# Optimization experiments

Measured on AMD Instinct MI355X. Metric: run time of the kernel, lower is better.

The kernel has to match this reference:

```python
import jax, jax.numpy as jnp
import numpy as np

B, T, L, D, U = 2048, 500, 128, 64, 128  # batch, time steps, latent_dim, output_dim, n_units


def setup_inputs() -> dict:
    key = jax.random.key(0)
    ks = jax.random.split(key, 10)
    def init(k, shape, fan_in):
        return jax.random.uniform(k, shape, jnp.float32, -1.0, 1.0) / np.sqrt(fan_in)
    return {
        "first_point": jax.random.normal(ks[0], (1, B, L), jnp.float32),
        "time_steps_to_predict": jnp.arange(T, dtype=jnp.float32),
        # GRUCell params (torch layout: weight [3*hidden, in], gates ordered r,z,n)
        "w_ih": init(ks[1], (3 * L, D + 1), L),
        "w_hh": init(ks[2], (3 * L, L), L),
        "b_ih": init(ks[3], (3 * L,), L),
        "b_hh": init(ks[4], (3 * L,), L),
        # output_net: Linear(L,U) -> tanh -> Linear(U,D)
        "w1": init(ks[5], (U, L), L),
        "b1": jnp.zeros((U,), jnp.float32),
        "w2": init(ks[6], (D, U), U),
        "b2": jnp.zeros((D,), jnp.float32),
    }


def _gru_cell(x, h, w_ih, w_hh, b_ih, b_hh):
    gi = x @ w_ih.T + b_ih  # [B, 3L]
    gh = h @ w_hh.T + b_hh  # [B, 3L]
    i_r, i_z, i_n = jnp.split(gi, 3, axis=-1)
    h_r, h_z, h_n = jnp.split(gh, 3, axis=-1)
    r = jax.nn.sigmoid(i_r + h_r)
    z = jax.nn.sigmoid(i_z + h_z)
    n = jnp.tanh(i_n + r * h_n)
    return (1.0 - z) * n + z * h


def reference(first_point, time_steps_to_predict, w_ih, w_hh, b_ih, b_hh, w1, b1, w2, b2):
    def mlp(h):
        return jnp.tanh(h @ w1.T + b1) @ w2.T + b2  # [B, D]

    ts = time_steps_to_predict
    delta_ts = jnp.concatenate([jnp.zeros((1,), ts.dtype), ts[1:] - ts[:-1]])  # [T]

    h0 = first_point[0]          # [B, L]
    p0 = mlp(h0)                 # [B, D]
    batch = h0.shape[0]

    def step(carry, dt):
        h, p = carry
        dt_col = jnp.broadcast_to(dt.reshape(1, 1), (batch, 1))
        x = jnp.concatenate([p, dt_col], axis=-1)  # [B, D+1]
        h = _gru_cell(x, h, w_ih, w_hh, b_ih, b_hh)
        p = mlp(h)
        return (h, p), (h, p)

    _, (hs, ps) = jax.lax.scan(step, (h0, p0), delta_ts[1:])  # [T-1, B, *]
    sol_z = jnp.concatenate([h0[None], hs], axis=0)   # [T, B, L]
    pred_x = jnp.concatenate([p0[None], ps], axis=0)  # [T, B, D]
    sol_z = jnp.transpose(sol_z, (1, 0, 2))[None]     # [1, B, T, L]
    pred_x = jnp.transpose(pred_x, (1, 0, 2))[None]   # [1, B, T, D]
    return sol_z, pred_x
```

## Files before the change

kernel.cpp:

```cpp
#include <hip/hip_runtime.h>

#define BB 2048
#define TT 500
#define LL 128
#define DD 64
#define UU 128

using f16x8 = __attribute__((ext_vector_type(8))) _Float16;
using f32x4 = __attribute__((ext_vector_type(4))) float;

__device__ __forceinline__ float bf2f(unsigned short u){
  union { unsigned u; float f; } v; v.u = ((unsigned)u) << 16; return v.f;
}
__device__ __forceinline__ unsigned short f2bf(float f){
  union { float f; unsigned u; } v; v.f = f;
  unsigned r = v.u + 0x7FFFu + ((v.u >> 16) & 1u);
  return (unsigned short)(r >> 16);
}
__device__ __forceinline__ float cvt(unsigned short v){ return bf2f(v); }
__device__ __forceinline__ float cvt(float v){ return v; }

__device__ __forceinline__ float sigmoidf_(float x){
  return __builtin_amdgcn_rcpf(1.f + __expf(-x));
}
__device__ __forceinline__ float tanhf_(float x){
  float e = __expf(2.f * x);
  return 1.f - 2.f * __builtin_amdgcn_rcpf(1.f + e);
}

__device__ __forceinline__ void bar_lds(){
  asm volatile("s_waitcnt lgkmcnt(0)\n\ts_barrier" ::: "memory");
}

#define SH 136
#define SA 136

struct Frags {
  f16x8 Wc[3][4];
  f16x8 Wh[3][4];
  f16x8 W1f[4];
  f16x8 W2f[4];
  float br, bz, bin, bhn, wdr, wdz, wdn, b1c, b2c;
};

template <typename T>
__device__ __forceinline__ void preload(
    const void* wih_, const void* whh_, const void* bih_, const void* bhh_,
    const void* w1_, const void* b1_, const void* w2_, const void* b2_,
    int c, int lq, Frags& F)
{
  const T* wih = (const T*)wih_; const T* whh = (const T*)whh_;
  const T* bih = (const T*)bih_; const T* bhh = (const T*)bhh_;
  const T* w1  = (const T*)w1_;  const T* b1  = (const T*)b1_;
  const T* w2  = (const T*)w2_;  const T* b2  = (const T*)b2_;
  #pragma unroll
  for (int g = 0; g < 3; ++g){
    const int row = g*128 + c;
    #pragma unroll
    for (int kt = 0; kt < 4; ++kt)
      #pragma unroll
      for (int j = 0; j < 8; ++j)
        F.Wh[g][kt][j] = (_Float16)cvt(whh[row*128 + kt*32 + lq*8 + j]);
  }
  #pragma unroll
  for (int kt = 0; kt < 4; ++kt)
    #pragma unroll
    for (int j = 0; j < 8; ++j)
      F.W1f[kt][j] = (_Float16)cvt(w1[c*128 + kt*32 + lq*8 + j]);
  const int c2 = c & 63;
  #pragma unroll
  for (int kt = 0; kt < 4; ++kt)
    #pragma unroll
    for (int j = 0; j < 8; ++j)
      F.W2f[kt][j] = (_Float16)cvt(w2[c2*128 + kt*32 + lq*8 + j]);

  for (int kt = 0; kt < 4; ++kt){
    float acc[3][8];
    #pragma unroll
    for (int g = 0; g < 3; ++g)
      #pragma unroll
      for (int j = 0; j < 8; ++j) acc[g][j] = 0.f;
    for (int d = 0; d < 64; ++d){
      float w2r[8];
      #pragma unroll
      for (int j = 0; j < 8; ++j)
        w2r[j] = cvt(w2[d*128 + kt*32 + lq*8 + j]);
      #pragma unroll
      for (int g = 0; g < 3; ++g){
        const float wpv = cvt(wih[(g*128 + c)*65 + d]);
        #pragma unroll
        for (int j = 0; j < 8; ++j) acc[g][j] += wpv * w2r[j];
      }
    }
    #pragma unroll
    for (int g = 0; g < 3; ++g)
      #pragma unroll
      for (int j = 0; j < 8; ++j)
        F.Wc[g][kt][j] = (_Float16)acc[g][j];
  }
  float bc[3] = {0.f, 0.f, 0.f};
  for (int d = 0; d < 64; ++d){
    const float b2v = cvt(b2[d]);
    #pragma unroll
    for (int g = 0; g < 3; ++g)
      bc[g] += cvt(wih[(g*128 + c)*65 + d]) * b2v;
  }
  F.br  = cvt(bih[c])     + cvt(bhh[c])     + bc[0];
  F.bz  = cvt(bih[128+c]) + cvt(bhh[128+c]) + bc[1];
  F.bin = cvt(bih[256+c]) + bc[2];
  F.bhn = cvt(bhh[256+c]);
  F.wdr = cvt(wih[c*65 + 64]);
  F.wdz = cvt(wih[(128+c)*65 + 64]);
  F.wdn = cvt(wih[(256+c)*65 + 64]);
  F.b1c = cvt(b1[c]);
  F.b2c = cvt(b2[c2]);
}

__global__ __launch_bounds__(512, 2) void rnn_decoder(
    const void* __restrict__ fp0,
    const void* __restrict__ ts,
    const void* __restrict__ wih,
    const void* __restrict__ whh,
    const void* __restrict__ bih,
    const void* __restrict__ bhh,
    const void* __restrict__ w1,
    const void* __restrict__ b1,
    const void* __restrict__ w2,
    const void* __restrict__ b2,
    void* __restrict__ out)
{
  __shared__ __align__(16) _Float16 sh[16*SH];
  __shared__ __align__(16) _Float16 sa[16*SA];
  __shared__ float dts[TT];

  const int tid  = threadIdx.x;
  const int wv   = tid >> 6;
  const int lane = tid & 63;
  const int lm   = lane & 15;
  const int lq   = lane >> 4;
  const int b0   = blockIdx.x << 4;
  const int c    = (wv << 4) + lm;

  const bool isbf = (((const unsigned*)ts)[1] != 0x3F800000u);

  Frags F;
  if (isbf) preload<unsigned short>(wih, whh, bih, bhh, w1, b1, w2, b2, c, lq, F);
  else      preload<float>         (wih, whh, bih, bhh, w1, b1, w2, b2, c, lq, F);

  if (isbf){
    const unsigned short* t16 = (const unsigned short*)ts;
    for (int t = tid; t < TT; t += 512)
      dts[t] = t ? (bf2f(t16[t]) - bf2f(t16[t-1])) : 0.f;
  } else {
    const float* t32 = (const float*)ts;
    for (int t = tid; t < TT; t += 512)
      dts[t] = t ? (t32[t] - t32[t-1]) : 0.f;
  }

  unsigned short* outh16 = (unsigned short*)out;
  unsigned short* outp16 = outh16 + (size_t)BB*TT*LL;
  float* outh32 = (float*)out;
  float* outp32 = outh32 + (size_t)BB*TT*LL;

  {
    const int row = tid >> 5;
    const int k4  = (tid & 31) << 2;
    if (isbf){
      const unsigned short* src = (const unsigned short*)fp0 + (b0 + row)*LL + k4;
      ushort4 v = *(const ushort4*)src;
      #pragma unroll
      for (int j = 0; j < 4; ++j)
        sh[row*SH + k4 + j] = (_Float16)bf2f(((const unsigned short*)&v)[j]);
      *(ushort4*)(outh16 + (size_t)(b0 + row)*TT*LL + k4) = v;
    } else {
      const float* src = (const float*)fp0 + (b0 + row)*LL + k4;
      float4 v = *(const float4*)src;
      sh[row*SH + k4 + 0] = (_Float16)v.x;
      sh[row*SH + k4 + 1] = (_Float16)v.y;
      sh[row*SH + k4 + 2] = (_Float16)v.z;
      sh[row*SH + k4 + 3] = (_Float16)v.w;
      *(float4*)(outh32 + (size_t)(b0 + row)*TT*LL + k4) = v;
    }
  }
  bar_lds();

  float hprev[4];
  #pragma unroll
  for (int i = 0; i < 4; ++i)
    hprev[i] = (float)sh[(lq*4 + i)*SH + c];

  f16x8 ahc[4], aac[4];
  #pragma unroll
  for (int kt = 0; kt < 4; ++kt)
    ahc[kt] = *(const f16x8*)&sh[lm*SH + kt*32 + lq*8];

  {
    f32x4 acc = {0,0,0,0};
    #pragma unroll
    for (int kt = 0; kt < 4; ++kt)
      acc = __builtin_amdgcn_mfma_f32_16x16x32_f16(ahc[kt], F.W1f[kt], acc, 0,0,0);
    #pragma unroll
    for (int i = 0; i < 4; ++i)
      sa[(lq*4 + i)*SA + c] = (_Float16)tanhf_(acc[i] + F.b1c);
  }
  bar_lds();
  #pragma unroll
  for (int kt = 0; kt < 4; ++kt)
    aac[kt] = *(const f16x8*)&sa[lm*SA + kt*32 + lq*8];

  for (int t = 1; t < TT; ++t){
    const float dt = dts[t];
    f32x4 aR = {0,0,0,0}, aZ = {0,0,0,0}, aN = {0,0,0,0}, aH = {0,0,0,0};
    #pragma unroll
    for (int kt = 0; kt < 4; ++kt){
      aR = __builtin_amdgcn_mfma_f32_16x16x32_f16(aac[kt], F.Wc[0][kt], aR, 0,0,0);
      aZ = __builtin_amdgcn_mfma_f32_16x16x32_f16(aac[kt], F.Wc[1][kt], aZ, 0,0,0);
      aN = __builtin_amdgcn_mfma_f32_16x16x32_f16(aac[kt], F.Wc[2][kt], aN, 0,0,0);
      aH = __builtin_amdgcn_mfma_f32_16x16x32_f16(ahc[kt], F.Wh[2][kt], aH, 0,0,0);
    }
    #pragma unroll
    for (int kt = 0; kt < 4; ++kt){
      aR = __builtin_amdgcn_mfma_f32_16x16x32_f16(ahc[kt], F.Wh[0][kt], aR, 0,0,0);
      aZ = __builtin_amdgcn_mfma_f32_16x16x32_f16(ahc[kt], F.Wh[1][kt], aZ, 0,0,0);
    }
    f32x4 aP = {0,0,0,0};
    if (wv < 4){
      #pragma unroll
      for (int kt = 0; kt < 4; ++kt)
        aP = __builtin_amdgcn_mfma_f32_16x16x32_f16(aac[kt], F.W2f[kt], aP, 0,0,0);
    }
    float hnew[4];
    #pragma unroll
    for (int i = 0; i < 4; ++i){
      const float r = sigmoidf_(aR[i] + F.br + dt*F.wdr);
      const float z = sigmoidf_(aZ[i] + F.bz + dt*F.wdz);
      const float n = tanhf_(aN[i] + F.bin + dt*F.wdn + r*(aH[i] + F.bhn));
      hnew[i] = (1.f - z)*n + z*hprev[i];
      hprev[i] = hnew[i];
    }
    #pragma unroll
    for (int i = 0; i < 4; ++i)
      sh[(lq*4 + i)*SH + c] = (_Float16)hnew[i];
    bar_lds();
    #pragma unroll
    for (int kt = 0; kt < 4; ++kt)
      ahc[kt] = *(const f16x8*)&sh[lm*SH + kt*32 + lq*8];
    if (!isbf){
      #pragma unroll
      for (int i = 0; i < 4; ++i)
        outh32[(size_t)(b0 + lq*4 + i)*TT*LL + (size_t)t*LL + c] = hnew[i];
      if (wv < 4){
        #pragma unroll
        for (int i = 0; i < 4; ++i)
          outp32[(size_t)(b0 + lq*4 + i)*TT*DD + (size_t)(t-1)*DD + c] = aP[i] + F.b2c;
      }
    } else {
      #pragma unroll
      for (int i = 0; i < 4; ++i)
        outh16[(size_t)(b0 + lq*4 + i)*TT*LL + (size_t)t*LL + c] = f2bf(hnew[i]);
      if (wv < 4){
        #pragma unroll
        for (int i = 0; i < 4; ++i)
          outp16[(size_t)(b0 + lq*4 + i)*TT*DD + (size_t)(t-1)*DD + c] = f2bf(aP[i] + F.b2c);
      }
    }
    {
      f32x4 acc = {0,0,0,0};
      #pragma unroll
      for (int kt = 0; kt < 4; ++kt)
        acc = __builtin_amdgcn_mfma_f32_16x16x32_f16(ahc[kt], F.W1f[kt], acc, 0,0,0);
      #pragma unroll
      for (int i = 0; i < 4; ++i)
        sa[(lq*4 + i)*SA + c] = (_Float16)tanhf_(acc[i] + F.b1c);
    }
    bar_lds();
    #pragma unroll
    for (int kt = 0; kt < 4; ++kt)
      aac[kt] = *(const f16x8*)&sa[lm*SA + kt*32 + lq*8];
  }

  if (wv < 4){
    f32x4 aP = {0,0,0,0};
    #pragma unroll
    for (int kt = 0; kt < 4; ++kt)
      aP = __builtin_amdgcn_mfma_f32_16x16x32_f16(aac[kt], F.W2f[kt], aP, 0,0,0);
    if (!isbf){
      #pragma unroll
      for (int i = 0; i < 4; ++i)
        outp32[(size_t)(b0 + lq*4 + i)*TT*DD + (size_t)(TT-1)*DD + c] = aP[i] + F.b2c;
    } else {
      #pragma unroll
      for (int i = 0; i < 4; ++i)
        outp16[(size_t)(b0 + lq*4 + i)*TT*DD + (size_t)(TT-1)*DD + c] = f2bf(aP[i] + F.b2c);
    }
  }
}

extern "C" void kernel_launch(void* const* d_in, const int* in_sizes, int n_in,
                              void* d_out, int out_size, void* d_ws, size_t ws_size,
                              hipStream_t stream) {
  (void)in_sizes; (void)n_in; (void)out_size; (void)d_ws; (void)ws_size;
  rnn_decoder<<<dim3(BB/16), dim3(512), 0, stream>>>(
      d_in[0],
      d_in[1],
      d_in[2],
      d_in[3],
      d_in[4],
      d_in[5],
      d_in[6],
      d_in[7],
      d_in[8],
      d_in[9],
      d_out);
}
```

Baseline: 1.342 ms.

## Fold exp2 scaling into weights, move hidden GEMMs off the critical path, precompute output offsets

The log2(e) factors of sigmoid and tanh are folded into the preloaded weights and biases, so each activation becomes a raw v_exp_f32 plus a reciprocal with no multiply. The hidden-state MFMAs (r, z, n gates) for the next step now run right after the new h is read back, alongside the W1 MLP, rather than at the start of the next step, shortening the dependency chain between the two barriers. Output addresses are held as incremented 32-bit offsets instead of being recomputed each step. Scaling weights before the fp16 conversion changes rounding slightly, and 32-bit offsets assume the output index stays within range.

```diff
diff --git a/kernel.cpp b/kernel.cpp
--- a/kernel.cpp
+++ b/kernel.cpp
@@ -20,17 +20,16 @@
 __device__ __forceinline__ float cvt(unsigned short v){ return bf2f(v); }
 __device__ __forceinline__ float cvt(float v){ return v; }
 
-__device__ __forceinline__ float sigmoidf_(float x){
-  return __builtin_amdgcn_rcpf(1.f + __expf(-x));
-}
-__device__ __forceinline__ float tanhf_(float x){
-  float e = __expf(2.f * x);
-  return 1.f - 2.f * __builtin_amdgcn_rcpf(1.f + e);
+__device__ __forceinline__ float exp2_(float x){
+  float r; asm("v_exp_f32 %0, %1" : "=v"(r) : "v"(x)); return r;
 }
 
 __device__ __forceinline__ void bar_lds(){
   asm volatile("s_waitcnt lgkmcnt(0)\n\ts_barrier" ::: "memory");
 }
+
+#define C1 (-1.44269504088896340736f)
+#define C2 ( 2.88539008177792681472f)
 
 #define SH 136
 #define SA 136
@@ -53,6 +52,7 @@
   const T* bih = (const T*)bih_; const T* bhh = (const T*)bhh_;
   const T* w1  = (const T*)w1_;  const T* b1  = (const T*)b1_;
   const T* w2  = (const T*)w2_;  const T* b2  = (const T*)b2_;
+  const float gs[3] = {C1, C1, C2};
   #pragma unroll
   for (int g = 0; g < 3; ++g){
     const int row = g*128 + c;
@@ -60,13 +60,13 @@
     for (int kt = 0; kt < 4; ++kt)
       #pragma unroll
       for (int j = 0; j < 8; ++j)
-        F.Wh[g][kt][j] = (_Float16)cvt(whh[row*128 + kt*32 + lq*8 + j]);
+        F.Wh[g][kt][j] = (_Float16)(gs[g]*cvt(whh[row*128 + kt*32 + lq*8 + j]));
   }
   #pragma unroll
   for (int kt = 0; kt < 4; ++kt)
     #pragma unroll
     for (int j = 0; j < 8; ++j)
-      F.W1f[kt][j] = (_Float16)cvt(w1[c*128 + kt*32 + lq*8 + j]);
+      F.W1f[kt][j] = (_Float16)(C2*cvt(w1[c*128 + kt*32 + lq*8 + j]));
   const int c2 = c & 63;
   #pragma unroll
   for (int kt = 0; kt < 4; ++kt)
@@ -96,7 +96,7 @@
     for (int g = 0; g < 3; ++g)
       #pragma unroll
       for (int j = 0; j < 8; ++j)
-        F.Wc[g][kt][j] = (_Float16)acc[g][j];
+        F.Wc[g][kt][j] = (_Float16)(gs[g]*acc[g][j]);
   }
   float bc[3] = {0.f, 0.f, 0.f};
   for (int d = 0; d < 64; ++d){
@@ -105,14 +105,14 @@
     for (int g = 0; g < 3; ++g)
       bc[g] += cvt(wih[(g*128 + c)*65 + d]) * b2v;
   }
-  F.br  = cvt(bih[c])     + cvt(bhh[c])     + bc[0];
-  F.bz  = cvt(bih[128+c]) + cvt(bhh[128+c]) + bc[1];
-  F.bin = cvt(bih[256+c]) + bc[2];
-  F.bhn = cvt(bhh[256+c]);
-  F.wdr = cvt(wih[c*65 + 64]);
-  F.wdz = cvt(wih[(128+c)*65 + 64]);
-  F.wdn = cvt(wih[(256+c)*65 + 64]);
-  F.b1c = cvt(b1[c]);
+  F.br  = C1*(cvt(bih[c])     + cvt(bhh[c])     + bc[0]);
+  F.bz  = C1*(cvt(bih[128+c]) + cvt(bhh[128+c]) + bc[1]);
+  F.bin = C2*(cvt(bih[256+c]) + bc[2]);
+  F.bhn = C2*cvt(bhh[256+c]);
+  F.wdr = C1*cvt(wih[c*65 + 64]);
+  F.wdz = C1*cvt(wih[(128+c)*65 + 64]);
+  F.wdn = C2*cvt(wih[(256+c)*65 + 64]);
+  F.b1c = C2*cvt(b1[c]);
   F.b2c = cvt(b2[c2]);
 }
 
@@ -162,6 +162,13 @@
   float* outh32 = (float*)out;
   float* outp32 = outh32 + (size_t)BB*TT*LL;
 
+  unsigned offh[4], offp[4];
+  #pragma unroll
+  for (int i = 0; i < 4; ++i){
+    offh[i] = (unsigned)((b0 + lq*4 + i)*TT*LL + c) + (unsigned)LL;
+    offp[i] = (unsigned)((b0 + lq*4 + i)*TT*DD + (c & 63));
+  }
+
   {
     const int row = tid >> 5;
     const int k4  = (tid & 31) << 2;
@@ -194,14 +201,22 @@
   for (int kt = 0; kt < 4; ++kt)
     ahc[kt] = *(const f16x8*)&sh[lm*SH + kt*32 + lq*8];
 
+  f32x4 aR = {0,0,0,0}, aZ = {0,0,0,0}, aH = {0,0,0,0};
   {
     f32x4 acc = {0,0,0,0};
     #pragma unroll
     for (int kt = 0; kt < 4; ++kt)
       acc = __builtin_amdgcn_mfma_f32_16x16x32_f16(ahc[kt], F.W1f[kt], acc, 0,0,0);
     #pragma unroll
+    for (int kt = 0; kt < 4; ++kt){
+      aR = __builtin_amdgcn_mfma_f32_16x16x32_f16(ahc[kt], F.Wh[0][kt], aR, 0,0,0);
+      aZ = __builtin_amdgcn_mfma_f32_16x16x32_f16(ahc[kt], F.Wh[1][kt], aZ, 0,0,0);
+      aH = __builtin_amdgcn_mfma_f32_16x16x32_f16(ahc[kt], F.Wh[2][kt], aH, 0,0,0);
+    }
+    #pragma unroll
     for (int i = 0; i < 4; ++i)
-      sa[(lq*4 + i)*SA + c] = (_Float16)tanhf_(acc[i] + F.b1c);
+      sa[(lq*4 + i)*SA + c] =
+        (_Float16)(1.f - 2.f*__builtin_amdgcn_rcpf(1.f + exp2_(acc[i] + F.b1c)));
   }
   bar_lds();
   #pragma unroll
@@ -210,69 +225,75 @@
 
   for (int t = 1; t < TT; ++t){
     const float dt = dts[t];
-    f32x4 aR = {0,0,0,0}, aZ = {0,0,0,0}, aN = {0,0,0,0}, aH = {0,0,0,0};
+    f32x4 aN = {0,0,0,0};
     #pragma unroll
     for (int kt = 0; kt < 4; ++kt){
       aR = __builtin_amdgcn_mfma_f32_16x16x32_f16(aac[kt], F.Wc[0][kt], aR, 0,0,0);
       aZ = __builtin_amdgcn_mfma_f32_16x16x32_f16(aac[kt], F.Wc[1][kt], aZ, 0,0,0);
       aN = __builtin_amdgcn_mfma_f32_16x16x32_f16(aac[kt], F.Wc[2][kt], aN, 0,0,0);
-      aH = __builtin_amdgcn_mfma_f32_16x16x32_f16(ahc[kt], F.Wh[2][kt], aH, 0,0,0);
-    }
+    }
+    f32x4 aP = {0,0,0,0};
+    if (wv < 4){
+      #pragma unroll
+      for (int kt = 0; kt < 4; ++kt)
+        aP = __builtin_amdgcn_mfma_f32_16x16x32_f16(aac[kt], F.W2f[kt], aP, 0,0,0);
+    }
+    const float rb = F.br + dt*F.wdr;
+    const float zb = F.bz + dt*F.wdz;
+    const float nb = F.bin + dt*F.wdn;
+    float hnew[4];
+    #pragma unroll
+    for (int i = 0; i < 4; ++i){
+      const float r = __builtin_amdgcn_rcpf(1.f + exp2_(aR[i] + rb));
+      const float z = __builtin_amdgcn_rcpf(1.f + exp2_(aZ[i] + zb));
+      const float y = aN[i] + nb + r*(aH[i] + F.bhn);
+      const float n = 1.f - 2.f*__builtin_amdgcn_rcpf(1.f + exp2_(y));
+      hnew[i] = n + z*(hprev[i] - n);
+      hprev[i] = hnew[i];
+    }
+    #pragma unroll
+    for (int i = 0; i < 4; ++i)
+      sh[(lq*4 + i)*SH + c] = (_Float16)hnew[i];
+    bar_lds();
+    #pragma unroll
+    for (int kt = 0; kt < 4; ++kt)
+      ahc[kt] = *(const f16x8*)&sh[lm*SH + kt*32 + lq*8];
+    f32x4 acc = {0,0,0,0};
+    #pragma unroll
+    for (int kt = 0; kt < 4; ++kt)
+      acc = __builtin_amdgcn_mfma_f32_16x16x32_f16(ahc[kt], F.W1f[kt], acc, 0,0,0);
+    if (!isbf){
+      #pragma unroll
+      for (int i = 0; i < 4; ++i)
+        outh32[offh[i]] = hnew[i];
+      if (wv < 4){
+        #pragma unroll
+        for (int i = 0; i < 4; ++i)
+          outp32[offp[i]] = aP[i] + F.b2c;
+      }
+    } else {
+      #pragma unroll
+      for (int i = 0; i < 4; ++i)
+        outh16[offh[i]] = f2bf(hnew[i]);
+      if (wv < 4){
+        #pragma unroll
+        for (int i = 0; i < 4; ++i)
+          outp16[offp[i]] = f2bf(aP[i] + F.b2c);
+      }
+    }
+    #pragma unroll
+    for (int i = 0; i < 4; ++i){ offh[i] += LL; offp[i] += DD; }
+    aR = (f32x4){0,0,0,0}; aZ = (f32x4){0,0,0,0}; aH = (f32x4){0,0,0,0};
     #pragma unroll
     for (int kt = 0; kt < 4; ++kt){
       aR = __builtin_amdgcn_mfma_f32_16x16x32_f16(ahc[kt], F.Wh[0][kt], aR, 0,0,0);
       aZ = __builtin_amdgcn_mfma_f32_16x16x32_f16(ahc[kt], F.Wh[1][kt], aZ, 0,0,0);
-    }
-    f32x4 aP = {0,0,0,0};
-    if (wv < 4){
-      #pragma unroll
-      for (int kt = 0; kt < 4; ++kt)
-        aP = __builtin_amdgcn_mfma_f32_16x16x32_f16(aac[kt], F.W2f[kt], aP, 0,0,0);
-    }
-    float hnew[4];
-    #pragma unroll
-    for (int i = 0; i < 4; ++i){
-      const float r = sigmoidf_(aR[i] + F.br + dt*F.wdr);
-      const float z = sigmoidf_(aZ[i] + F.bz + dt*F.wdz);
-      const float n = tanhf_(aN[i] + F.bin + dt*F.wdn + r*(aH[i] + F.bhn));
-      hnew[i] = (1.f - z)*n + z*hprev[i];
-      hprev[i] = hnew[i];
+      aH = __builtin_amdgcn_mfma_f32_16x16x32_f16(ahc[kt], F.Wh[2][kt], aH, 0,0,0);
     }
     #pragma unroll
     for (int i = 0; i < 4; ++i)
-      sh[(lq*4 + i)*SH + c] = (_Float16)hnew[i];
-    bar_lds();
-    #pragma unroll
-    for (int kt = 0; kt < 4; ++kt)
-      ahc[kt] = *(const f16x8*)&sh[lm*SH + kt*32 + lq*8];
-    if (!isbf){
-      #pragma unroll
-      for (int i = 0; i < 4; ++i)
-        outh32[(size_t)(b0 + lq*4 + i)*TT*LL + (size_t)t*LL + c] = hnew[i];
-      if (wv < 4){
-        #pragma unroll
-        for (int i = 0; i < 4; ++i)
-          outp32[(size_t)(b0 + lq*4 + i)*TT*DD + (size_t)(t-1)*DD + c] = aP[i] + F.b2c;
-      }
-    } else {
-      #pragma unroll
-      for (int i = 0; i < 4; ++i)
-        outh16[(size_t)(b0 + lq*4 + i)*TT*LL + (size_t)t*LL + c] = f2bf(hnew[i]);
-      if (wv < 4){
-        #pragma unroll
-        for (int i = 0; i < 4; ++i)
-          outp16[(size_t)(b0 + lq*4 + i)*TT*DD + (size_t)(t-1)*DD + c] = f2bf(aP[i] + F.b2c);
-      }
-    }
-    {
-      f32x4 acc = {0,0,0,0};
-      #pragma unroll
-      for (int kt = 0; kt < 4; ++kt)
-        acc = __builtin_amdgcn_mfma_f32_16x16x32_f16(ahc[kt], F.W1f[kt], acc, 0,0,0);
-      #pragma unroll
-      for (int i = 0; i < 4; ++i)
-        sa[(lq*4 + i)*SA + c] = (_Float16)tanhf_(acc[i] + F.b1c);
-    }
+      sa[(lq*4 + i)*SA + c] =
+        (_Float16)(1.f - 2.f*__builtin_amdgcn_rcpf(1.f + exp2_(acc[i] + F.b1c)));
     bar_lds();
     #pragma unroll
     for (int kt = 0; kt < 4; ++kt)
@@ -287,11 +308,11 @@
     if (!isbf){
       #pragma unroll
       for (int i = 0; i < 4; ++i)
-        outp32[(size_t)(b0 + lq*4 + i)*TT*DD + (size_t)(TT-1)*DD + c] = aP[i] + F.b2c;
+        outp32[offp[i]] = aP[i] + F.b2c;
     } else {
       #pragma unroll
       for (int i = 0; i < 4; ++i)
-        outp16[(size_t)(b0 + lq*4 + i)*TT*DD + (size_t)(TT-1)*DD + c] = f2bf(aP[i] + F.b2c);
+        outp16[offp[i]] = f2bf(aP[i] + F.b2c);
     }
   }
 }
```

New measurement: 1.297 ms. -3.3%, faster.

## Transpose MFMA operands for vectorized stores and fold exp2 scaling into weights

Applied to the files above, without the earlier changes.

Swaps the A/B operands of every MFMA so each lane owns four consecutive output columns for one batch row. LDS writes of h and the activations become single f16x4 stores, and global output writes become float4 or packed-bf16 vector stores with incrementing offsets. The sigmoid/tanh pre-scale constants (-log2e, 2log2e) are folded into the weights and biases so the gates can use a raw v_exp_f32, and the accumulator chains are split to shorten MFMA dependencies. The costs are per-lane bias arrays (more registers), a different LDS padding, and small fp16 rounding differences from the pre-scaled weights.

```diff
diff --git a/kernel.cpp b/kernel.cpp
--- a/kernel.cpp
+++ b/kernel.cpp
@@ -4,70 +4,70 @@
 #define TT 500
 #define LL 128
 #define DD 64
-#define UU 128
 
 using f16x8 = __attribute__((ext_vector_type(8))) _Float16;
+using f16x4 = __attribute__((ext_vector_type(4))) _Float16;
 using f32x4 = __attribute__((ext_vector_type(4))) float;
 
 __device__ __forceinline__ float bf2f(unsigned short u){
   union { unsigned u; float f; } v; v.u = ((unsigned)u) << 16; return v.f;
 }
-__device__ __forceinline__ unsigned short f2bf(float f){
-  union { float f; unsigned u; } v; v.f = f;
-  unsigned r = v.u + 0x7FFFu + ((v.u >> 16) & 1u);
-  return (unsigned short)(r >> 16);
-}
 __device__ __forceinline__ float cvt(unsigned short v){ return bf2f(v); }
 __device__ __forceinline__ float cvt(float v){ return v; }
 
-__device__ __forceinline__ float sigmoidf_(float x){
-  return __builtin_amdgcn_rcpf(1.f + __expf(-x));
-}
-__device__ __forceinline__ float tanhf_(float x){
-  float e = __expf(2.f * x);
-  return 1.f - 2.f * __builtin_amdgcn_rcpf(1.f + e);
+__device__ __forceinline__ unsigned pkbf(float lo, float hi){
+  unsigned r;
+  asm("v_cvt_pk_bf16_f32 %0, %1, %2" : "=v"(r) : "v"(lo), "v"(hi));
+  return r;
+}
+
+__device__ __forceinline__ float exp2_(float x){
+  float r; asm("v_exp_f32 %0, %1" : "=v"(r) : "v"(x)); return r;
 }
 
 __device__ __forceinline__ void bar_lds(){
   asm volatile("s_waitcnt lgkmcnt(0)\n\ts_barrier" ::: "memory");
 }
 
-#define SH 136
-#define SA 136
+#define C1 (-1.44269504088896340736f)
+#define C2 ( 2.88539008177792681472f)
+
+#define SHW 152
 
 struct Frags {
   f16x8 Wc[3][4];
   f16x8 Wh[3][4];
   f16x8 W1f[4];
   f16x8 W2f[4];
-  float br, bz, bin, bhn, wdr, wdz, wdn, b1c, b2c;
+  float br[4], bz[4], bin[4], bhn[4], wdr[4], wdz[4], wdn[4], b1c[4], b2c[4];
 };
 
 template <typename T>
 __device__ __forceinline__ void preload(
     const void* wih_, const void* whh_, const void* bih_, const void* bhh_,
     const void* w1_, const void* b1_, const void* w2_, const void* b2_,
-    int c, int lq, Frags& F)
+    int cA, int lq, int cD, Frags& F)
 {
   const T* wih = (const T*)wih_; const T* whh = (const T*)whh_;
   const T* bih = (const T*)bih_; const T* bhh = (const T*)bhh_;
   const T* w1  = (const T*)w1_;  const T* b1  = (const T*)b1_;
   const T* w2  = (const T*)w2_;  const T* b2  = (const T*)b2_;
+  const float gs[3] = {C1, C1, C2};
   #pragma unroll
   for (int g = 0; g < 3; ++g){
-    const int row = g*128 + c;
+    const int row = g*128 + cA;
     #pragma unroll
     for (int kt = 0; kt < 4; ++kt)
       #pragma unroll
       for (int j = 0; j < 8; ++j)
-        F.Wh[g][kt][j] = (_Float16)cvt(whh[row*128 + kt*32 + lq*8 + j]);
+        F.Wh[g][kt][j] = (_Float16)(gs[g]*cvt(whh[row*128 + kt*32 + lq*8 + j]));
   }
   #pragma unroll
   for (int kt = 0; kt < 4; ++kt)
     #pragma unroll
     for (int j = 0; j < 8; ++j)
-      F.W1f[kt][j] = (_Float16)cvt(w1[c*128 + kt*32 + lq*8 + j]);
-  const int c2 = c & 63;
+      F.W1f[kt][j] = (_Float16)(C2*cvt(w1[cA*128 + kt*32 + lq*8 + j]));
+  const int c2 = cA & 63;
   #pragma unroll
   for (int kt = 0; kt < 4; ++kt)
     #pragma unroll
@@ -87,7 +87,7 @@
         w2r[j] = cvt(w2[d*128 + kt*32 + lq*8 + j]);
       #pragma unroll
       for (int g = 0; g < 3; ++g){
-        const float wpv = cvt(wih[(g*128 + c)*65 + d]);
+        const float wpv = cvt(wih[(g*128 + cA)*65 + d]);
         #pragma unroll
         for (int j = 0; j < 8; ++j) acc[g][j] += wpv * w2r[j];
       }
@@ -96,24 +96,28 @@
     for (int g = 0; g < 3; ++g)
       #pragma unroll
       for (int j = 0; j < 8; ++j)
-        F.Wc[g][kt][j] = (_Float16)acc[g][j];
-  }
-  float bc[3] = {0.f, 0.f, 0.f};
-  for (int d = 0; d < 64; ++d){
-    const float b2v = cvt(b2[d]);
-    #pragma unroll
-    for (int g = 0; g < 3; ++g)
-      bc[g] += cvt(wih[(g*128 + c)*65 + d]) * b2v;
-  }
-  F.br  = cvt(bih[c])     + cvt(bhh[c])     + bc[0];
-  F.bz  = cvt(bih[128+c]) + cvt(bhh[128+c]) + bc[1];
-  F.bin = cvt(bih[256+c]) + bc[2];
-  F.bhn = cvt(bhh[256+c]);
-  F.wdr = cvt(wih[c*65 + 64]);
-  F.wdz = cvt(wih[(128+c)*65 + 64]);
-  F.wdn = cvt(wih[(256+c)*65 + 64]);
-  F.b1c = cvt(b1[c]);
-  F.b2c = cvt(b2[c2]);
+        F.Wc[g][kt][j] = (_Float16)(gs[g]*acc[g][j]);
+  }
+  #pragma unroll
+  for (int i = 0; i < 4; ++i){
+    const int ci = cD + i;
+    float bc0 = 0.f, bc1 = 0.f, bc2 = 0.f;
+    for (int d = 0; d < 64; ++d){
+      const float b2v = cvt(b2[d]);
+      bc0 += cvt(wih[(      ci)*65 + d]) * b2v;
+      bc1 += cvt(wih[(128 + ci)*65 + d]) * b2v;
+      bc2 += cvt(wih[(256 + ci)*65 + d]) * b2v;
+    }
+    F.br[i]  = C1*(cvt(bih[ci])     + cvt(bhh[ci])     + bc0);
+    F.bz[i]  = C1*(cvt(bih[128+ci]) + cvt(bhh[128+ci]) + bc1);
+    F.bin[i] = C2*(cvt(bih[256+ci]) + bc2);
+    F.bhn[i] = C2*cvt(bhh[256+ci]);
+    F.wdr[i] = C1*cvt(wih[ci*65 + 64]);
+    F.wdz[i] = C1*cvt(wih[(128+ci)*65 + 64]);
+    F.wdn[i] = C2*cvt(wih[(256+ci)*65 + 64]);
+    F.b1c[i] = C2*cvt(b1[ci]);
+    F.b2c[i] = cvt(b2[ci & 63]);
+  }
 }
 
 __global__ __launch_bounds__(512, 2) void rnn_decoder(
@@ -129,8 +133,8 @@
     const void* __restrict__ b2,
     void* __restrict__ out)
 {
-  __shared__ __align__(16) _Float16 sh[16*SH];
-  __shared__ __align__(16) _Float16 sa[16*SA];
+  __shared__ __align__(16) _Float16 sh2[16*SHW];
+  __shared__ __align__(16) _Float16 sa2[16*SHW];
   __shared__ float dts[TT];
 
   const int tid  = threadIdx.x;
@@ -139,13 +143,14 @@
   const int lm   = lane & 15;
   const int lq   = lane >> 4;
   const int b0   = blockIdx.x << 4;
-  const int c    = (wv << 4) + lm;
+  const int cA   = (wv << 4) + lm;
+  const int cD   = (wv << 4) + (lq << 2);
 
   const bool isbf = (((const unsigned*)ts)[1] != 0x3F800000u);
 
   Frags F;
-  if (isbf) preload<unsigned short>(wih, whh, bih, bhh, w1, b1, w2, b2, c, lq, F);
-  else      preload<float>         (wih, whh, bih, bhh, w1, b1, w2, b2, c, lq, F);
+  if (isbf) preload<unsigned short>(wih, whh, bih, bhh, w1, b1, w2, b2, cA, lq, cD, F);
+  else      preload<float>         (wih, whh, bih, bhh, w1, b1, w2, b2, cA, lq, cD, F);
 
   if (isbf){
     const unsigned short* t16 = (const unsigned short*)ts;
@@ -162,136 +167,166 @@
   float* outh32 = (float*)out;
   float* outp32 = outh32 + (size_t)BB*TT*LL;
 
+  unsigned offh = (unsigned)((b0 + lm)*TT*LL + cD) + (unsigned)LL;
+  unsigned offp = (unsigned)((b0 + lm)*TT*DD + (cD & 63));
+
   {
     const int row = tid >> 5;
     const int k4  = (tid & 31) << 2;
     if (isbf){
       const unsigned short* src = (const unsigned short*)fp0 + (b0 + row)*LL + k4;
       ushort4 v = *(const ushort4*)src;
+      f16x4 hv;
       #pragma unroll
       for (int j = 0; j < 4; ++j)
-        sh[row*SH + k4 + j] = (_Float16)bf2f(((const unsigned short*)&v)[j]);
+        hv[j] = (_Float16)bf2f(((const unsigned short*)&v)[j]);
+      *(f16x4*)&sh2[row*SHW + k4] = hv;
       *(ushort4*)(outh16 + (size_t)(b0 + row)*TT*LL + k4) = v;
     } else {
       const float* src = (const float*)fp0 + (b0 + row)*LL + k4;
       float4 v = *(const float4*)src;
-      sh[row*SH + k4 + 0] = (_Float16)v.x;
-      sh[row*SH + k4 + 1] = (_Float16)v.y;
-      sh[row*SH + k4 + 2] = (_Float16)v.z;
-      sh[row*SH + k4 + 3] = (_Float16)v.w;
+      f16x4 hv;
+      hv[0] = (_Float16)v.x; hv[1] = (_Float16)v.y;
+      hv[2] = (_Float16)v.z; hv[3] = (_Float16)v.w;
+      *(f16x4*)&sh2[row*SHW + k4] = hv;
       *(float4*)(outh32 + (size_t)(b0 + row)*TT*LL + k4) = v;
     }
   }
   bar_lds();
 
   float hprev[4];
-  #pragma unroll
-  for (int i = 0; i < 4; ++i)
-    hprev[i] = (float)sh[(lq*4 + i)*SH + c];
+  {
+    f16x4 hv = *(const f16x4*)&sh2[lm*SHW + cD];
+    #pragma unroll
+    for (int i = 0; i < 4; ++i) hprev[i] = (float)hv[i];
+  }
 
   f16x8 ahc[4], aac[4];
   #pragma unroll
   for (int kt = 0; kt < 4; ++kt)
-    ahc[kt] = *(const f16x8*)&sh[lm*SH + kt*32 + lq*8];
+    ahc[kt] = *(const f16x8*)&sh2[lm*SHW + kt*32 + lq*8];
 
   {
-    f32x4 acc = {0,0,0,0};
-    #pragma unroll
-    for (int kt = 0; kt < 4; ++kt)
-      acc = __builtin_amdgcn_mfma_f32_16x16x32_f16(ahc[kt], F.W1f[kt], acc, 0,0,0);
+    f32x4 a0 = {0,0,0,0}, a1v = {0,0,0,0};
+    a0  = __builtin_amdgcn_mfma_f32_16x16x32_f16(F.W1f[0], ahc[0], a0, 0,0,0);
+    a1v = __builtin_amdgcn_mfma_f32_16x16x32_f16(F.W1f[1], ahc[1], a1v, 0,0,0);
+    a0  = __builtin_amdgcn_mfma_f32_16x16x32_f16(F.W1f[2], ahc[2], a0, 0,0,0);
+    a1v = __builtin_amdgcn_mfma_f32_16x16x32_f16(F.W1f[3], ahc[3], a1v, 0,0,0);
+    f16x4 av;
     #pragma unroll
     for (int i = 0; i < 4; ++i)
-      sa[(lq*4 + i)*SA + c] = (_Float16)tanhf_(acc[i] + F.b1c);
+      av[i] = (_Float16)(1.f - 2.f*__builtin_amdgcn_rcpf(1.f + exp2_(a0[i] + a1v[i] + F.b1c[i])));
+    *(f16x4*)&sa2[lm*SHW + cD] = av;
   }
   bar_lds();
   #pragma unroll
   for (int kt = 0; kt < 4; ++kt)
-    aac[kt] = *(const f16x8*)&sa[lm*SA + kt*32 + lq*8];
+    aac[kt] = *(const f16x8*)&sa2[lm*SHW + kt*32 + lq*8];
 
   for (int t = 1; t < TT; ++t){
     const float dt = dts[t];
-    f32x4 aR = {0,0,0,0}, aZ = {0,0,0,0}, aN = {0,0,0,0}, aH = {0,0,0,0};
+    float rb[4], zb[4], nb[4];
+    #pragma unroll
+    for (int i = 0; i < 4; ++i){
+      rb[i] = F.br[i]  + dt*F.wdr[i];
+      zb[i] = F.bz[i]  + dt*F.wdz[i];
+      nb[i] = F.bin[i] + dt*F.wdn[i];
+    }
+    f32x4 aRh = {0,0,0,0}, aZh = {0,0,0,0}, aH = {0,0,0,0};
     #pragma unroll
     for (int kt = 0; kt < 4; ++kt){
-      aR = __builtin_amdgcn_mfma_f32_16x16x32_f16(aac[kt], F.Wc[0][kt], aR, 0,0,0);
-      aZ = __builtin_amdgcn_mfma_f32_16x16x32_f16(aac[kt], F.Wc[1][kt], aZ, 0,0,0);
-      aN = __builtin_amdgcn_mfma_f32_16x16x32_f16(aac[kt], F.Wc[2][kt], aN, 0,0,0);
-      aH = __builtin_amdgcn_mfma_f32_16x16x32_f16(ahc[kt], F.Wh[2][kt], aH, 0,0,0);
-    }
+      aRh = __builtin_amdgcn_mfma_f32_16x16x32_f16(F.Wh[0][kt], ahc[kt], aRh, 0,0,0);
+      aZh = __builtin_amdgcn_mfma_f32_16x16x32_f16(F.Wh[1][kt], ahc[kt], aZh, 0,0,0);
+      aH  = __builtin_amdgcn_mfma_f32_16x16x32_f16(F.Wh[2][kt], ahc[kt], aH, 0,0,0);
+    }
+    f32x4 aRc = {0,0,0,0}, aZc = {0,0,0,0}, aN = {0,0,0,0};
     #pragma unroll
     for (int kt = 0; kt < 4; ++kt){
-      aR = __builtin_amdgcn_mfma_f32_16x16x32_f16(ahc[kt], F.Wh[0][kt], aR, 0,0,0);
-      aZ = __builtin_amdgcn_mfma_f32_16x16x32_f16(ahc[kt], F.Wh[1][kt], aZ, 0,0,0);
+      aRc = __builtin_amdgcn_mfma_f32_16x16x32_f16(F.Wc[0][kt], aac[kt], aRc, 0,0,0);
+      aZc = __builtin_amdgcn_mfma_f32_16x16x32_f16(F.Wc[1][kt], aac[kt], aZc, 0,0,0);
+      aN  = __builtin_amdgcn_mfma_f32_16x16x32_f16(F.Wc[2][kt], aac[kt], aN, 0,0,0);
     }
     f32x4 aP = {0,0,0,0};
     if (wv < 4){
       #pragma unroll
       for (int kt = 0; kt < 4; ++kt)
-        aP = __builtin_amdgcn_mfma_f32_16x16x32_f16(aac[kt], F.W2f[kt], aP, 0,0,0);
+        aP = __builtin_amdgcn_mfma_f32_16x16x32_f16(F.W2f[kt], aac[kt], aP, 0,0,0);
     }
     float hnew[4];
     #pragma unroll
     for (int i = 0; i < 4; ++i){
-      const float r = sigmoidf_(aR[i] + F.br + dt*F.wdr);
-      const float z = sigmoidf_(aZ[i] + F.bz + dt*F.wdz);
-      const float n = tanhf_(aN[i] + F.bin + dt*F.wdn + r*(aH[i] + F.bhn));
-      hnew[i] = (1.f - z)*n + z*hprev[i];
+      const float r = __builtin_amdgcn_rcpf(1.f + exp2_(aRh[i] + aRc[i] + rb[i]));
+      const float z = __builtin_amdgcn_rcpf(1.f + exp2_(aZh[i] + aZc[i] + zb[i]));
+      const float y = aN[i] + nb[i] + r*(aH[i] + F.bhn[i]);
+      const float n = 1.f - 2.f*__builtin_amdgcn_rcpf(1.f + exp2_(y));
+      hnew[i] = n + z*(hprev[i] - n);
       hprev[i] = hnew[i];
     }
-    #pragma unroll
-    for (int i = 0; i < 4; ++i)
-      sh[(lq*4 + i)*SH + c] = (_Float16)hnew[i];
+    {
+      f16x4 hv;
+      #pragma unroll
+      for (int i = 0; i < 4; ++i) hv[i] = (_Float16)hnew[i];
+      *(f16x4*)&sh2[lm*SHW + cD] = hv;
+    }
     bar_lds();
     #pragma unroll
     for (int kt = 0; kt < 4; ++kt)
-      ahc[kt] = *(const f16x8*)&sh[lm*SH + kt*32 + lq*8];
+      ahc[kt] = *(const f16x8*)&sh2[lm*SHW + kt*32 + lq*8];
     if (!isbf){
-      #pragma unroll
-      for (int i = 0; i < 4; ++i)
-        outh32[(size_t)(b0 + lq*4 + i)*TT*LL + (size_t)t*LL + c] = hnew[i];
+      float4 hv4; hv4.x = hnew[0]; hv4.y = hnew[1]; hv4.z = hnew[2]; hv4.w = hnew[3];
+      *(float4*)(outh32 + offh) = hv4;
       if (wv < 4){
-        #pragma unroll
-        for (int i = 0; i < 4; ++i)
-          outp32[(size_t)(b0 + lq*4 + i)*TT*DD + (size_t)(t-1)*DD + c] = aP[i] + F.b2c;
+        float4 pv4;
+        pv4.x = aP[0] + F.b2c[0]; pv4.y = aP[1] + F.b2c[1];
+        pv4.z = aP[2] + F.b2c[2]; pv4.w = aP[3] + F.b2c[3];
+        *(float4*)(outp32 + offp) = pv4;
       }
     } else {
+      uint2 hb;
+      hb.x = pkbf(hnew[0], hnew[1]);
+      hb.y = pkbf(hnew[2], hnew[3]);
+      *(uint2*)(outh16 + offh) = hb;
+      if (wv < 4){
+        uint2 pb;
+        pb.x = pkbf(aP[0] + F.b2c[0], aP[1] + F.b2c[1]);
+        pb.y = pkbf(aP[2] + F.b2c[2], aP[3] + F.b2c[3]);
+        *(uint2*)(outp16 + offp) = pb;
+      }
+    }
+    offh += LL; offp += DD;
+    {
+      f32x4 a0 = {0,0,0,0}, a1v = {0,0,0,0};
+      a0  = __builtin_amdgcn_mfma_f32_16x16x32_f16(F.W1f[0], ahc[0], a0, 0,0,0);
+      a1v = __builtin_amdgcn_mfma_f32_16x16x32_f16(F.W1f[1], ahc[1], a1v, 0,0,0);
+      a0  = __builtin_amdgcn_mfma_f32_16x16x32_f16(F.W1f[2], ahc[2], a0, 0,0,0);
+      a1v = __builtin_amdgcn_mfma_f32_16x16x32_f16(F.W1f[3], ahc[3], a1v, 0,0,0);
+      f16x4 av;
       #pragma unroll
       for (int i = 0; i < 4; ++i)
-        outh16[(size_t)(b0 + lq*4 + i)*TT*LL + (size_t)t*LL + c] = f2bf(hnew[i]);
-      if (wv < 4){
-        #pragma unroll
-        for (int i = 0; i < 4; ++i)
-          outp16[(size_t)(b0 + lq*4 + i)*TT*DD + (size_t)(t-1)*DD + c] = f2bf(aP[i] + F.b2c);
-      }
-    }
-    {
-      f32x4 acc = {0,0,0,0};
-      #pragma unroll
-      for (int kt = 0; kt < 4; ++kt)
-        acc = __builtin_amdgcn_mfma_f32_16x16x32_f16(ahc[kt], F.W1f[kt], acc, 0,0,0);
-      #pragma unroll
-      for (int i = 0; i < 4; ++i)
-        sa[(lq*4 + i)*SA + c] = (_Float16)tanhf_(acc[i] + F.b1c);
+        av[i] = (_Float16)(1.f - 2.f*__builtin_amdgcn_rcpf(1.f + exp2_(a0[i] + a1v[i] + F.b1c[i])));
+      *(f16x4*)&sa2[lm*SHW + cD] = av;
     }
     bar_lds();
     #pragma unroll
     for (int kt = 0; kt < 4; ++kt)
-      aac[kt] = *(const f16x8*)&sa[lm*SA + kt*32 + lq*8];
+      aac[kt] = *(const f16x8*)&sa2[lm*SHW + kt*32 + lq*8];
   }
 
   if (wv < 4){
     f32x4 aP = {0,0,0,0};
     #pragma unroll
     for (int kt = 0; kt < 4; ++kt)
-      aP = __builtin_amdgcn_mfma_f32_16x16x32_f16(aac[kt], F.W2f[kt], aP, 0,0,0);
+      aP = __builtin_amdgcn_mfma_f32_16x16x32_f16(F.W2f[kt], aac[kt], aP, 0,0,0);
     if (!isbf){
-      #pragma unroll
-      for (int i = 0; i < 4; ++i)
-        outp32[(size_t)(b0 + lq*4 + i)*TT*DD + (size_t)(TT-1)*DD + c] = aP[i] + F.b2c;
+      float4 pv4;
+      pv4.x = aP[0] + F.b2c[0]; pv4.y = aP[1] + F.b2c[1];
+      pv4.z = aP[2] + F.b2c[2]; pv4.w = aP[3] + F.b2c[3];
+      *(float4*)(outp32 + offp) = pv4;
     } else {
-      #pragma unroll
-      for (int i = 0; i < 4; ++i)
-        outp16[(size_t)(b0 + lq*4 + i)*TT*DD + (size_t)(TT-1)*DD + c] = f2bf(aP[i] + F.b2c);
+      uint2 pb;
+      pb.x = pkbf(aP[0] + F.b2c[0], aP[1] + F.b2c[1]);
+      pb.y = pkbf(aP[2] + F.b2c[2], aP[3] + F.b2c[3]);
+      *(uint2*)(outp16 + offp) = pb;
     }
   }
 }
```

New measurement: 1.326 ms. About the same (-1.2%).
